# Kernel tuning notes

Hardware: AMD Instinct MI355X
Metric: run time of the kernel (lower is better)

Reference implementation:

```python
import jax, jax.numpy as jnp
import numpy as np

B, N, E, H, ET = 1, 50000, 600000, 128, 8
EPS = 1e-5


def setup_inputs() -> dict:
    key = jax.random.key(0)
    ks = jax.random.split(key, 20)
    s = 1.0 / np.sqrt(H)
    s2 = 1.0 / np.sqrt(2 * H)
    u = lambda k, shape, b: jax.random.uniform(k, shape, jnp.float32, -b, b)
    return {
        "hidden": jax.random.normal(ks[0], (B, N, H), jnp.float32),
        "edge_index": jax.random.randint(ks[1], (2, E), 0, N),
        "edge_type": jax.random.randint(ks[2], (E,), 0, ET),
        "edge_emb": jax.random.normal(ks[3], (ET, H), jnp.float32),
        "Wq": u(ks[4], (H, H), s), "bq": u(ks[5], (H,), s),
        "Wk": u(ks[6], (H, H), s), "bk": u(ks[7], (H,), s),
        "Wv": u(ks[8], (H, H), s), "bv": u(ks[9], (H,), s),
        "Web": u(ks[10], (H, 1), s), "beb": u(ks[11], (1,), s),
        "W1": u(ks[12], (2 * H, H), s2), "b1": u(ks[13], (H,), s2),
        "W2": u(ks[14], (H, H), s), "b2": u(ks[15], (H,), s),
        "gamma": jnp.ones((H,), jnp.float32),
        "beta": jnp.zeros((H,), jnp.float32),
    }


def reference(hidden, edge_index, edge_type, edge_emb, Wq, bq, Wk, bk, Wv, bv,
              Web, beb, W1, b1, W2, b2, gamma, beta):
    source, target = edge_index[0], edge_index[1]
    src_h = hidden[:, source]                      # [B,E,H] gather
    tgt_h = hidden[:, target]                      # [B,E,H] gather
    eh = edge_emb[edge_type]                       # [E,H]

    q = tgt_h @ Wq + bq                            # [B,E,H]
    sk = src_h + eh[None]                          # [B,E,H]
    k = sk @ Wk + bk
    v = sk @ Wv + bv

    logits = (q * k).sum(-1) / np.sqrt(H)          # [B,E]
    logits = logits + (eh @ Web + beb)[:, 0][None] # edge bias, same across batch

    # segment softmax over incoming edges per target node
    lt = logits.T                                  # [E,B]
    mx = jax.ops.segment_max(lt, target, num_segments=N)   # [N,B]
    ex = jnp.exp(lt - mx[target])
    sm = jax.ops.segment_sum(ex, target, num_segments=N)   # [N,B]
    w = (ex / sm[target]).T                        # [B,E]

    messages = v * w[..., None]                    # [B,E,H]
    agg = jax.ops.segment_sum(jnp.moveaxis(messages, 1, 0), target,
                              num_segments=N)      # [N,B,H]
    agg = jnp.moveaxis(agg, 0, 1)                  # [B,N,H]

    h = jnp.concatenate([hidden, agg], axis=-1)    # [B,N,2H]
    upd = jax.nn.silu(h @ W1 + b1) @ W2 + b2

    x = hidden + upd
    mu = x.mean(-1, keepdims=True)
    var = ((x - mu) ** 2).mean(-1, keepdims=True)
    return (x - mu) / jnp.sqrt(var + EPS) * gamma + beta
```

## Files before the change

kernel.cpp:

```cpp
#include <hip/hip_runtime.h>
#include <math.h>

#define NN 50000
#define NPAD 50048
#define NE 600000
#define H 128
#define ET 8
#define EPS 1e-5f
#define INVSQ 0.08838834764831845f

typedef __attribute__((ext_vector_type(8))) short bf16x8;
typedef __attribute__((ext_vector_type(8))) unsigned short u16x8;
typedef __attribute__((ext_vector_type(4))) float f32x4;

static __device__ inline float bf_lo(unsigned int w) { return __uint_as_float(w << 16); }
static __device__ inline float bf_hi(unsigned int w) { return __uint_as_float(w & 0xFFFF0000u); }
static __device__ inline float bfu(unsigned short v) {
  return __uint_as_float((unsigned int)v << 16);
}
static __device__ inline unsigned short f2bf(float f) {
  unsigned int u = __float_as_uint(f);
  return (unsigned short)((u + 0x7FFFu + ((u >> 16) & 1u)) >> 16);
}

#define PH_B 3125
#define PW_B 384
#define ET_B 8
#define HIST_B 2344

__global__ __launch_bounds__(256) void prep_all_kernel(
    const float* __restrict__ hidden, const float* __restrict__ edge_emb,
    const float* __restrict__ Wq, const float* __restrict__ Wk, const float* __restrict__ Wv,
    const float* __restrict__ W1, const float* __restrict__ W2,
    const float* __restrict__ Web, const float* __restrict__ beb,
    const int* __restrict__ tgt,
    unsigned short* __restrict__ hcat, unsigned short* __restrict__ WqkvT,
    unsigned short* __restrict__ W1T, unsigned short* __restrict__ W2T,
    float* __restrict__ Kef, float* __restrict__ Vef, float* __restrict__ ebuf,
    int* __restrict__ deg) {
  const int blk = blockIdx.x;
  const int t = threadIdx.x;
  if (blk < PH_B) {
    int g = blk * 256 + t;
    int row = g >> 4, seg = g & 15;
    const float4* src = (const float4*)(hidden + (size_t)row * 128 + seg * 8);
    float4 x0 = src[0], x1 = src[1];
    u16x8 o;
    o[0] = f2bf(x0.x); o[1] = f2bf(x0.y); o[2] = f2bf(x0.z); o[3] = f2bf(x0.w);
    o[4] = f2bf(x1.x); o[5] = f2bf(x1.y); o[6] = f2bf(x1.z); o[7] = f2bf(x1.w);
    *(u16x8*)(hcat + (size_t)row * 256 + seg * 8) = o;
  } else if (blk < PH_B + PW_B) {
    int idx = (blk - PH_B) * 256 + t;
    if (idx < 49152) {
      int r = idx >> 7, k = idx & 127;
      const float* W = (r < 128) ? Wq : (r < 256) ? Wk : Wv;
      WqkvT[idx] = f2bf(W[k * 128 + (r & 127)]);
    } else if (idx < 81920) {
      int j = idx - 49152;
      int r = j >> 8, k = j & 255;
      W1T[j] = f2bf(W1[k * 128 + r]);
    } else if (idx < 98304) {
      int j = idx - 81920;
      int r = j >> 7, k = j & 127;
      W2T[j] = f2bf(W2[k * 128 + r]);
    }
  } else if (blk < PH_B + PW_B + ET_B) {
    int e = blk - (PH_B + PW_B);
    if (t < 128) {
      float sk = 0.f, sv = 0.f;
      for (int i = 0; i < 128; ++i) {
        float ev = edge_emb[e * 128 + i];
        sk = fmaf(ev, Wk[i * 128 + t], sk);
        sv = fmaf(ev, Wv[i * 128 + t], sv);
      }
      Kef[e * 128 + t] = sk;
      Vef[e * 128 + t] = sv;
    } else if (t == 128) {
      float s2 = beb[0];
      for (int i = 0; i < 128; ++i) s2 = fmaf(edge_emb[e * 128 + i], Web[i], s2);
      ebuf[e] = s2;
    }
  } else {
    int e = (blk - (PH_B + PW_B + ET_B)) * 256 + t;
    if (e < NE) atomicAdd(&deg[tgt[e]], 1);
  }
}

__global__ __launch_bounds__(256) void qkv_mfma_kernel(
    const unsigned short* __restrict__ hcat, const unsigned short* __restrict__ WqkvT,
    const float* __restrict__ bq, const float* __restrict__ bk, const float* __restrict__ bv,
    unsigned short* __restrict__ Qb, unsigned short* __restrict__ KV_u16) {
  __shared__ unsigned short stage[64][392];
  const int tid = threadIdx.x;
  const int w = tid >> 6, l = tid & 63;
  const int lr = l & 15, lg = l >> 4;
  const int blk = blockIdx.x;

  f32x4 acc[4][6] = {};
  const unsigned short* Ab = hcat + (size_t)(blk * 64 + lr) * 256 + lg * 8;
  const unsigned short* Bb = WqkvT + (size_t)(w * 96 + lr) * 128 + lg * 8;
#pragma unroll
  for (int ks = 0; ks < 4; ++ks) {
    bf16x8 a[4];
#pragma unroll
    for (int mt = 0; mt < 4; ++mt) a[mt] = *(const bf16x8*)(Ab + mt * 16 * 256 + ks * 32);
#pragma unroll
    for (int ct = 0; ct < 6; ++ct) {
      bf16x8 b = *(const bf16x8*)(Bb + ct * 16 * 128 + ks * 32);
#pragma unroll
      for (int mt = 0; mt < 4; ++mt)
        acc[mt][ct] = __builtin_amdgcn_mfma_f32_16x16x32_bf16(a[mt], b, acc[mt][ct], 0, 0, 0);
    }
  }
#pragma unroll
  for (int ct = 0; ct < 6; ++ct) {
    int c = w * 96 + ct * 16 + lr;
    float bias = (c < 128) ? bq[c] : (c < 256) ? bk[c - 128] : bv[c - 256];
    float sc = (c < 128) ? INVSQ : 1.f;
    int off;
    if (c < 128) off = c;
    else if (c < 256) { int j = c - 128; off = 128 + ((j >> 1) << 2) + (j & 1); }
    else { int j = c - 256; off = 128 + ((j >> 1) << 2) + 2 + (j & 1); }
#pragma unroll
    for (int mt = 0; mt < 4; ++mt)
#pragma unroll
      for (int j = 0; j < 4; ++j)
        stage[mt * 16 + lg * 4 + j][off] = f2bf((acc[mt][ct][j] + bias) * sc);
  }
  __syncthreads();
  for (int idx = tid; idx < 64 * 48; idx += 256) {
    int r = idx / 48, g = idx % 48;
    int row = blk * 64 + r;
    if (row >= NN) continue;
    u16x8 v = *(const u16x8*)(&stage[r][g * 8]);
    if (g < 16) *(u16x8*)(Qb + (size_t)row * 128 + g * 8) = v;
    else *(u16x8*)(KV_u16 + (size_t)row * 256 + (g - 16) * 8) = v;
  }
}

__global__ __launch_bounds__(256) void qke_kernel(const unsigned short* __restrict__ Qb,
                                                  const float* __restrict__ Kef,
                                                  const float* __restrict__ ebuf,
                                                  float* __restrict__ qke) {
  const int wid = (blockIdx.x * 256 + threadIdx.x) >> 6;
  const int lane = threadIdx.x & 63;
  const int et = lane >> 3, part = lane & 7;
  const unsigned short* q = Qb + (size_t)wid * 128 + part * 16;
  u16x8 q0 = *(const u16x8*)q;
  u16x8 q1 = *(const u16x8*)(q + 8);
  const float4* kf = (const float4*)(Kef + et * 128 + part * 16);
  float4 k0 = kf[0], k1 = kf[1], k2 = kf[2], k3 = kf[3];
  float d = 0.f;
  d = fmaf(bfu(q0[0]), k0.x, d); d = fmaf(bfu(q0[1]), k0.y, d);
  d = fmaf(bfu(q0[2]), k0.z, d); d = fmaf(bfu(q0[3]), k0.w, d);
  d = fmaf(bfu(q0[4]), k1.x, d); d = fmaf(bfu(q0[5]), k1.y, d);
  d = fmaf(bfu(q0[6]), k1.z, d); d = fmaf(bfu(q0[7]), k1.w, d);
  d = fmaf(bfu(q1[0]), k2.x, d); d = fmaf(bfu(q1[1]), k2.y, d);
  d = fmaf(bfu(q1[2]), k2.z, d); d = fmaf(bfu(q1[3]), k2.w, d);
  d = fmaf(bfu(q1[4]), k3.x, d); d = fmaf(bfu(q1[5]), k3.y, d);
  d = fmaf(bfu(q1[6]), k3.z, d); d = fmaf(bfu(q1[7]), k3.w, d);
#pragma unroll
  for (int o = 4; o >= 1; o >>= 1) d += __shfl_xor(d, o);
  if (part == 0) qke[(size_t)wid * 8 + et] = d + ebuf[et];
}

__global__ __launch_bounds__(256) void scan1_kernel(const int* __restrict__ deg,
                                                    int* __restrict__ excl,
                                                    int* __restrict__ sums) {
  __shared__ int buf[256];
  int idx = blockIdx.x * 256 + threadIdx.x;
  int v = (idx < NN) ? deg[idx] : 0;
  buf[threadIdx.x] = v;
  __syncthreads();
  for (int o = 1; o < 256; o <<= 1) {
    int tv = (threadIdx.x >= o) ? buf[threadIdx.x - o] : 0;
    __syncthreads();
    buf[threadIdx.x] += tv;
    __syncthreads();
  }
  if (idx < NN) excl[idx] = buf[threadIdx.x] - v;
  if (threadIdx.x == 255) sums[blockIdx.x] = buf[255];
}

__global__ __launch_bounds__(256) void scan2_kernel(int* __restrict__ sums, int nb) {
  __shared__ int buf[256];
  int v = (threadIdx.x < nb) ? sums[threadIdx.x] : 0;
  buf[threadIdx.x] = v;
  __syncthreads();
  for (int o = 1; o < 256; o <<= 1) {
    int tv = (threadIdx.x >= o) ? buf[threadIdx.x - o] : 0;
    __syncthreads();
    buf[threadIdx.x] += tv;
    __syncthreads();
  }
  if (threadIdx.x < nb) sums[threadIdx.x] = buf[threadIdx.x] - v;
}

__global__ __launch_bounds__(256) void scan3_kernel(const int* __restrict__ excl,
                                                    const int* __restrict__ sums,
                                                    int* __restrict__ row_off,
                                                    int* __restrict__ cursor) {
  int idx = blockIdx.x * 256 + threadIdx.x;
  if (idx < NN) {
    int r = excl[idx] + sums[blockIdx.x];
    row_off[idx] = r;
    cursor[idx] = r;
  }
  if (idx == 0) row_off[NN] = NE;
}

__global__ void scatter_kernel(const int* __restrict__ src, const int* __restrict__ tgt,
                               const int* __restrict__ et, int* __restrict__ cursor,
                               int* __restrict__ packed) {
  int e = blockIdx.x * blockDim.x + threadIdx.x;
  if (e < NE) {
    int pos = atomicAdd(&cursor[tgt[e]], 1);
    packed[pos] = src[e] | (et[e] << 16);
  }
}

__global__ __launch_bounds__(256) void attn_kernel(
    const unsigned short* __restrict__ Qb, const uint4* __restrict__ KV4,
    const float* __restrict__ qke, const float* __restrict__ Vef,
    const int* __restrict__ row_off, const int* __restrict__ packed,
    unsigned short* __restrict__ hcat_u16) {
  const int wid = (blockIdx.x * blockDim.x + threadIdx.x) >> 6;
  const int lane = threadIdx.x & 63;
  const int g = lane >> 4, m = lane & 15;
  const int beg = row_off[wid], end = row_off[wid + 1];
  u16x8 qv = *(const u16x8*)(Qb + (size_t)wid * 128 + m * 8);
  float q[8];
#pragma unroll
  for (int j = 0; j < 8; ++j) q[j] = bfu(qv[j]);
  const float* qkb = qke + (size_t)wid * 8;
  float a[8] = {0.f, 0.f, 0.f, 0.f, 0.f, 0.f, 0.f, 0.f};
  float s = 0.f;
  for (int i = beg; i < end; i += 4) {
    int ii = i + g;
    bool valid = ii < end;
    int p = packed[valid ? ii : beg];
    int src = p & 0xFFFF, et = p >> 16;
    const uint4* row = KV4 + (size_t)src * 32 + m * 2;
    uint4 x0 = row[0], x1 = row[1];
    float d;
    d = bf_lo(x0.x) * q[0];
    d = fmaf(bf_hi(x0.x), q[1], d);
    d = fmaf(bf_lo(x0.z), q[2], d);
    d = fmaf(bf_hi(x0.z), q[3], d);
    d = fmaf(bf_lo(x1.x), q[4], d);
    d = fmaf(bf_hi(x1.x), q[5], d);
    d = fmaf(bf_lo(x1.z), q[6], d);
    d = fmaf(bf_hi(x1.z), q[7], d);
#pragma unroll
    for (int o = 8; o >= 1; o >>= 1) d += __shfl_xor(d, o);
    float pe = __expf(d + qkb[et]);
    pe = valid ? pe : 0.f;
    s += pe;
    const float4* vef = (const float4*)(Vef + et * 128 + m * 8);
    float4 v0 = vef[0], v1 = vef[1];
    a[0] = fmaf(pe, bf_lo(x0.y) + v0.x, a[0]);
    a[1] = fmaf(pe, bf_hi(x0.y) + v0.y, a[1]);
    a[2] = fmaf(pe, bf_lo(x0.w) + v0.z, a[2]);
    a[3] = fmaf(pe, bf_hi(x0.w) + v0.w, a[3]);
    a[4] = fmaf(pe, bf_lo(x1.y) + v1.x, a[4]);
    a[5] = fmaf(pe, bf_hi(x1.y) + v1.y, a[5]);
    a[6] = fmaf(pe, bf_lo(x1.w) + v1.z, a[6]);
    a[7] = fmaf(pe, bf_hi(x1.w) + v1.w, a[7]);
  }
#pragma unroll
  for (int o = 16; o <= 32; o <<= 1) {
    s += __shfl_xor(s, o);
#pragma unroll
    for (int j = 0; j < 8; ++j) a[j] += __shfl_xor(a[j], o);
  }
  if (g == 0) {
    float inv = (s > 0.f) ? 1.f / s : 0.f;
    u16x8 o;
#pragma unroll
    for (int j = 0; j < 8; ++j) o[j] = f2bf(a[j] * inv);
    *(u16x8*)(hcat_u16 + (size_t)wid * 256 + 128 + m * 8) = o;
  }
}

__global__ __launch_bounds__(256) void ffn_mfma_kernel(
    const unsigned short* __restrict__ hcat, const float* __restrict__ hidden,
    const unsigned short* __restrict__ W1T, const unsigned short* __restrict__ W2T,
    const float* __restrict__ b1, const float* __restrict__ b2,
    const float* __restrict__ gamma, const float* __restrict__ beta,
    float* __restrict__ out) {
  __shared__ unsigned short mid[64][136];
  const int tid = threadIdx.x;
  const int w = tid >> 6, l = tid & 63;
  const int lr = l & 15, lg = l >> 4;
  const int m0 = blockIdx.x * 64 + w * 16;

  f32x4 acc[8] = {};
  const unsigned short* Ab = hcat + (size_t)(m0 + lr) * 256 + lg * 8;
  const unsigned short* Bb = W1T + (size_t)lr * 256 + lg * 8;
#pragma unroll
  for (int ks = 0; ks < 8; ++ks) {
    bf16x8 a = *(const bf16x8*)(Ab + ks * 32);
#pragma unroll
    for (int ct = 0; ct < 8; ++ct) {
      bf16x8 b = *(const bf16x8*)(Bb + ct * 16 * 256 + ks * 32);
      acc[ct] = __builtin_amdgcn_mfma_f32_16x16x32_bf16(a, b, acc[ct], 0, 0, 0);
    }
  }
#pragma unroll
  for (int ct = 0; ct < 8; ++ct) {
    int c = ct * 16 + lr;
    float bb = b1[c];
#pragma unroll
    for (int j = 0; j < 4; ++j) {
      float x = acc[ct][j] + bb;
      float sl = x / (1.f + __expf(-x));
      mid[w * 16 + lg * 4 + j][c] = f2bf(sl);
    }
  }
  __syncthreads();

  f32x4 acc2[8] = {};
  const unsigned short* A2 = &mid[w * 16 + lr][0] + lg * 8;
  const unsigned short* B2 = W2T + (size_t)lr * 128 + lg * 8;
#pragma unroll
  for (int ks = 0; ks < 4; ++ks) {
    bf16x8 a = *(const bf16x8*)(A2 + ks * 32);
#pragma unroll
    for (int ct = 0; ct < 8; ++ct) {
      bf16x8 b = *(const bf16x8*)(B2 + ct * 16 * 128 + ks * 32);
      acc2[ct] = __builtin_amdgcn_mfma_f32_16x16x32_bf16(a, b, acc2[ct], 0, 0, 0);
    }
  }

  float ga[8], be[8], x[8][4];
#pragma unroll
  for (int ct = 0; ct < 8; ++ct) {
    int c = ct * 16 + lr;
    ga[ct] = gamma[c];
    be[ct] = beta[c];
    float bb = b2[c];
#pragma unroll
    for (int j = 0; j < 4; ++j) {
      int r = m0 + lg * 4 + j;
      float h = (r < NN) ? hidden[(size_t)r * 128 + c] : 0.f;
      x[ct][j] = acc2[ct][j] + bb + h;
    }
  }
#pragma unroll
  for (int j = 0; j < 4; ++j) {
    float s = 0.f, ss = 0.f;
#pragma unroll
    for (int ct = 0; ct < 8; ++ct) {
      s += x[ct][j];
      ss += x[ct][j] * x[ct][j];
    }
#pragma unroll
    for (int o = 8; o >= 1; o >>= 1) {
      s += __shfl_xor(s, o);
      ss += __shfl_xor(ss, o);
    }
    float mu = s * (1.f / 128.f);
    float inv = rsqrtf(ss * (1.f / 128.f) - mu * mu + EPS);
    int r = m0 + lg * 4 + j;
    if (r < NN) {
#pragma unroll
      for (int ct = 0; ct < 8; ++ct) {
        int c = ct * 16 + lr;
        out[(size_t)r * 128 + c] = (x[ct][j] - mu) * inv * ga[ct] + be[ct];
      }
    }
  }
}

extern "C" void kernel_launch(void* const* d_in, const int* in_sizes, int n_in,
                              void* d_out, int out_size, void* d_ws, size_t ws_size,
                              hipStream_t stream) {
  const float* hidden = (const float*)d_in[0];
  const int* edge_index = (const int*)d_in[1];
  const int* edge_type = (const int*)d_in[2];
  const float* edge_emb = (const float*)d_in[3];
  const float* Wq = (const float*)d_in[4];
  const float* bq = (const float*)d_in[5];
  const float* Wk = (const float*)d_in[6];
  const float* bk = (const float*)d_in[7];
  const float* Wv = (const float*)d_in[8];
  const float* bv = (const float*)d_in[9];
  const float* Web = (const float*)d_in[10];
  const float* beb = (const float*)d_in[11];
  const float* W1 = (const float*)d_in[12];
  const float* b1 = (const float*)d_in[13];
  const float* W2 = (const float*)d_in[14];
  const float* b2 = (const float*)d_in[15];
  const float* gamma = (const float*)d_in[16];
  const float* beta = (const float*)d_in[17];
  float* out = (float*)d_out;

  const int* srcp = edge_index;
  const int* tgtp = edge_index + NE;

  size_t off = 0;
  auto alloc = [&](size_t bytes) {
    void* p = (char*)d_ws + off;
    off += (bytes + 255) & ~(size_t)255;
    return p;
  };
  unsigned short* hcat = (unsigned short*)alloc((size_t)NPAD * 256 * 2);
  unsigned short* Qb = (unsigned short*)alloc((size_t)NPAD * 128 * 2);
  unsigned short* KV = (unsigned short*)alloc((size_t)NPAD * 256 * 2);
  unsigned short* WqkvT = (unsigned short*)alloc(384 * 128 * 2);
  unsigned short* W1T = (unsigned short*)alloc(128 * 256 * 2);
  unsigned short* W2T = (unsigned short*)alloc(128 * 128 * 2);
  float* Kef = (float*)alloc(ET * H * 4);
  float* Vef = (float*)alloc(ET * H * 4);
  float* ebuf = (float*)alloc(ET * 4);
  float* qke = (float*)alloc((size_t)NN * 8 * 4);
  int* deg = (int*)alloc((size_t)NN * 4);
  int* excl = (int*)alloc((size_t)NN * 4);
  int* sums = (int*)alloc(256 * 4);
  int* row_off = (int*)alloc((size_t)(NN + 1) * 4);
  int* cursor = (int*)alloc((size_t)NN * 4);
  int* packed = (int*)alloc((size_t)NE * 4);

  hipMemsetAsync(deg, 0, (size_t)NN * 4, stream);

  const int scan_blocks = (NN + 255) / 256;

  prep_all_kernel<<<PH_B + PW_B + ET_B + HIST_B, 256, 0, stream>>>(
      hidden, edge_emb, Wq, Wk, Wv, W1, W2, Web, beb, tgtp, hcat, WqkvT, W1T, W2T, Kef, Vef,
      ebuf, deg);
  scan1_kernel<<<scan_blocks, 256, 0, stream>>>(deg, excl, sums);
  scan2_kernel<<<1, 256, 0, stream>>>(sums, scan_blocks);
  scan3_kernel<<<scan_blocks, 256, 0, stream>>>(excl, sums, row_off, cursor);
  scatter_kernel<<<(NE + 255) / 256, 256, 0, stream>>>(srcp, tgtp, edge_type, cursor, packed);
  qkv_mfma_kernel<<<NPAD / 64, 256, 0, stream>>>(hcat, WqkvT, bq, bk, bv, Qb, KV);
  qke_kernel<<<NN / 4, 256, 0, stream>>>(Qb, Kef, ebuf, qke);
  attn_kernel<<<(NN * 64) / 256, 256, 0, stream>>>(Qb, (const uint4*)KV, qke, Vef, row_off,
                                                   packed, hcat);
  ffn_mfma_kernel<<<NPAD / 64, 256, 0, stream>>>(hcat, hidden, W1T, W2T, b1, b2, gamma, beta,
                                                 out);
}
```

Baseline: 333.3 us.

## Persistent FFN kernel with LDS-staged swizzled weights; split QKV tile across 8 waves

The FFN kernel becomes persistent with 256 blocks of 512 threads. Each block loads W1 and W2 once into swizzled LDS and its waves loop over 16-row tiles, each using a per-wave mid buffer. This removes the repeated global and L2 weight reads every block did before. The QKV kernel moves to 512 threads, with each wave computing a 32x96 tile instead of 64x96, which lowers register pressure and gives more waves per tile. The trade-off is about 100KB of LDS per FFN block, which limits occupancy, plus an explicit lgkmcnt wait in place of a block barrier.

```diff
diff --git a/kernel.cpp b/kernel.cpp
--- a/kernel.cpp
+++ b/kernel.cpp
@@ -3,6 +3,7 @@
 
 #define NN 50000
 #define NPAD 50048
+#define NTILES 3128
 #define NE 600000
 #define H 128
 #define ET 8
@@ -86,35 +87,34 @@
   }
 }
 
-__global__ __launch_bounds__(256) void qkv_mfma_kernel(
+__global__ __launch_bounds__(512) void qkv_mfma_kernel(
     const unsigned short* __restrict__ hcat, const unsigned short* __restrict__ WqkvT,
     const float* __restrict__ bq, const float* __restrict__ bk, const float* __restrict__ bv,
     unsigned short* __restrict__ Qb, unsigned short* __restrict__ KV_u16) {
   __shared__ unsigned short stage[64][392];
   const int tid = threadIdx.x;
   const int w = tid >> 6, l = tid & 63;
+  const int wr = w >> 2, wc = w & 3;
   const int lr = l & 15, lg = l >> 4;
   const int blk = blockIdx.x;
 
-  f32x4 acc[4][6] = {};
-  const unsigned short* Ab = hcat + (size_t)(blk * 64 + lr) * 256 + lg * 8;
-  const unsigned short* Bb = WqkvT + (size_t)(w * 96 + lr) * 128 + lg * 8;
+  f32x4 acc[2][6] = {};
+  const unsigned short* Ab = hcat + (size_t)(blk * 64 + wr * 32 + lr) * 256 + lg * 8;
+  const unsigned short* Bb = WqkvT + (size_t)(wc * 96 + lr) * 128 + lg * 8;
 #pragma unroll
   for (int ks = 0; ks < 4; ++ks) {
-    bf16x8 a[4];
-#pragma unroll
-    for (int mt = 0; mt < 4; ++mt) a[mt] = *(const bf16x8*)(Ab + mt * 16 * 256 + ks * 32);
+    bf16x8 a0 = *(const bf16x8*)(Ab + ks * 32);
+    bf16x8 a1 = *(const bf16x8*)(Ab + 16 * 256 + ks * 32);
 #pragma unroll
     for (int ct = 0; ct < 6; ++ct) {
       bf16x8 b = *(const bf16x8*)(Bb + ct * 16 * 128 + ks * 32);
-#pragma unroll
-      for (int mt = 0; mt < 4; ++mt)
-        acc[mt][ct] = __builtin_amdgcn_mfma_f32_16x16x32_bf16(a[mt], b, acc[mt][ct], 0, 0, 0);
+      acc[0][ct] = __builtin_amdgcn_mfma_f32_16x16x32_bf16(a0, b, acc[0][ct], 0, 0, 0);
+      acc[1][ct] = __builtin_amdgcn_mfma_f32_16x16x32_bf16(a1, b, acc[1][ct], 0, 0, 0);
     }
   }
 #pragma unroll
   for (int ct = 0; ct < 6; ++ct) {
-    int c = w * 96 + ct * 16 + lr;
+    int c = wc * 96 + ct * 16 + lr;
     float bias = (c < 128) ? bq[c] : (c < 256) ? bk[c - 128] : bv[c - 256];
     float sc = (c < 128) ? INVSQ : 1.f;
     int off;
@@ -122,13 +122,13 @@
     else if (c < 256) { int j = c - 128; off = 128 + ((j >> 1) << 2) + (j & 1); }
     else { int j = c - 256; off = 128 + ((j >> 1) << 2) + 2 + (j & 1); }
 #pragma unroll
-    for (int mt = 0; mt < 4; ++mt)
+    for (int mt = 0; mt < 2; ++mt)
 #pragma unroll
       for (int j = 0; j < 4; ++j)
-        stage[mt * 16 + lg * 4 + j][off] = f2bf((acc[mt][ct][j] + bias) * sc);
+        stage[wr * 32 + mt * 16 + lg * 4 + j][off] = f2bf((acc[mt][ct][j] + bias) * sc);
   }
   __syncthreads();
-  for (int idx = tid; idx < 64 * 48; idx += 256) {
+  for (int idx = tid; idx < 64 * 48; idx += 512) {
     int r = idx / 48, g = idx % 48;
     int row = blk * 64 + r;
     if (row >= NN) continue;
@@ -282,91 +282,128 @@
   }
 }
 
-__global__ __launch_bounds__(256) void ffn_mfma_kernel(
+__global__ __launch_bounds__(512) void ffn_mfma_kernel(
     const unsigned short* __restrict__ hcat, const float* __restrict__ hidden,
     const unsigned short* __restrict__ W1T, const unsigned short* __restrict__ W2T,
     const float* __restrict__ b1, const float* __restrict__ b2,
     const float* __restrict__ gamma, const float* __restrict__ beta,
     float* __restrict__ out) {
-  __shared__ unsigned short mid[64][136];
+  __shared__ unsigned short w1s[32768];
+  __shared__ unsigned short w2s[16384];
+  __shared__ unsigned short mids[8][2176];
   const int tid = threadIdx.x;
   const int w = tid >> 6, l = tid & 63;
   const int lr = l & 15, lg = l >> 4;
-  const int m0 = blockIdx.x * 64 + w * 16;
-
-  f32x4 acc[8] = {};
-  const unsigned short* Ab = hcat + (size_t)(m0 + lr) * 256 + lg * 8;
-  const unsigned short* Bb = W1T + (size_t)lr * 256 + lg * 8;
-#pragma unroll
-  for (int ks = 0; ks < 8; ++ks) {
-    bf16x8 a = *(const bf16x8*)(Ab + ks * 32);
-#pragma unroll
-    for (int ct = 0; ct < 8; ++ct) {
-      bf16x8 b = *(const bf16x8*)(Bb + ct * 16 * 256 + ks * 32);
-      acc[ct] = __builtin_amdgcn_mfma_f32_16x16x32_bf16(a, b, acc[ct], 0, 0, 0);
-    }
-  }
+
+#pragma unroll
+  for (int it = 0; it < 8; ++it) {
+    int idx = it * 512 + tid;
+    int c = idx >> 5, ks8 = idx & 31;
+    u16x8 v = *(const u16x8*)(W1T + c * 256 + ks8 * 8);
+    int byte = (c * 512 + ks8 * 16) ^ ((c & 7) << 4);
+    *(u16x8*)((char*)w1s + byte) = v;
+  }
+#pragma unroll
+  for (int it = 0; it < 4; ++it) {
+    int idx = it * 512 + tid;
+    int c = idx >> 4, ks8 = idx & 15;
+    u16x8 v = *(const u16x8*)(W2T + c * 128 + ks8 * 8);
+    int byte = (c * 256 + ks8 * 16) ^ ((c & 7) << 4);
+    *(u16x8*)((char*)w2s + byte) = v;
+  }
+  __syncthreads();
+
+  float bias1[8], bias2[8], ga[8], be[8];
 #pragma unroll
   for (int ct = 0; ct < 8; ++ct) {
     int c = ct * 16 + lr;
-    float bb = b1[c];
-#pragma unroll
-    for (int j = 0; j < 4; ++j) {
-      float x = acc[ct][j] + bb;
-      float sl = x / (1.f + __expf(-x));
-      mid[w * 16 + lg * 4 + j][c] = f2bf(sl);
-    }
-  }
-  __syncthreads();
-
-  f32x4 acc2[8] = {};
-  const unsigned short* A2 = &mid[w * 16 + lr][0] + lg * 8;
-  const unsigned short* B2 = W2T + (size_t)lr * 128 + lg * 8;
-#pragma unroll
-  for (int ks = 0; ks < 4; ++ks) {
-    bf16x8 a = *(const bf16x8*)(A2 + ks * 32);
-#pragma unroll
-    for (int ct = 0; ct < 8; ++ct) {
-      bf16x8 b = *(const bf16x8*)(B2 + ct * 16 * 128 + ks * 32);
-      acc2[ct] = __builtin_amdgcn_mfma_f32_16x16x32_bf16(a, b, acc2[ct], 0, 0, 0);
-    }
-  }
-
-  float ga[8], be[8], x[8][4];
-#pragma unroll
-  for (int ct = 0; ct < 8; ++ct) {
-    int c = ct * 16 + lr;
+    bias1[ct] = b1[c];
+    bias2[ct] = b2[c];
     ga[ct] = gamma[c];
     be[ct] = beta[c];
-    float bb = b2[c];
+  }
+  unsigned short* midw = mids[w];
+  const char* w1b = (const char*)w1s;
+  const char* w2b = (const char*)w2s;
+
+  for (int t = blockIdx.x * 8 + w; t < NTILES; t += 2048) {
+    const unsigned short* Ab = hcat + (size_t)(t * 16 + lr) * 256 + lg * 8;
+    bf16x8 a[8];
+#pragma unroll
+    for (int ks = 0; ks < 8; ++ks) a[ks] = *(const bf16x8*)(Ab + ks * 32);
+
+    f32x4 acc[8] = {};
+#pragma unroll
+    for (int ks = 0; ks < 8; ++ks) {
+#pragma unroll
+      for (int ct = 0; ct < 8; ++ct) {
+        int byte = ((ct * 16 + lr) * 512 + (lg * 8 + ks * 32) * 2) ^ ((lr & 7) << 4);
+        bf16x8 b = *(const bf16x8*)(w1b + byte);
+        acc[ct] = __builtin_amdgcn_mfma_f32_16x16x32_bf16(a[ks], b, acc[ct], 0, 0, 0);
+      }
+    }
+
+    float res[8][4];
+#pragma unroll
+    for (int ct = 0; ct < 8; ++ct)
+#pragma unroll
+      for (int j = 0; j < 4; ++j) {
+        int r = t * 16 + lg * 4 + j;
+        res[ct][j] = (r < NN) ? hidden[(size_t)r * 128 + ct * 16 + lr] : 0.f;
+      }
+
+#pragma unroll
+    for (int ct = 0; ct < 8; ++ct) {
+      float bb = bias1[ct];
+#pragma unroll
+      for (int j = 0; j < 4; ++j) {
+        float x = acc[ct][j] + bb;
+        float sl = x / (1.f + __expf(-x));
+        midw[(lg * 4 + j) * 136 + ct * 16 + lr] = f2bf(sl);
+      }
+    }
+    asm volatile("s_waitcnt lgkmcnt(0)" ::: "memory");
+    __builtin_amdgcn_sched_barrier(0);
+
+    f32x4 acc2[8] = {};
+#pragma unroll
+    for (int ks = 0; ks < 4; ++ks) {
+      bf16x8 a2 = *(const bf16x8*)(midw + lr * 136 + lg * 8 + ks * 32);
+#pragma unroll
+      for (int ct = 0; ct < 8; ++ct) {
+        int byte = ((ct * 16 + lr) * 256 + (lg * 8 + ks * 32) * 2) ^ ((lr & 7) << 4);
+        bf16x8 b = *(const bf16x8*)(w2b + byte);
+        acc2[ct] = __builtin_amdgcn_mfma_f32_16x16x32_bf16(a2, b, acc2[ct], 0, 0, 0);
+      }
+    }
+
+    float x[8][4];
+#pragma unroll
+    for (int ct = 0; ct < 8; ++ct)
+#pragma unroll
+      for (int j = 0; j < 4; ++j) x[ct][j] = acc2[ct][j] + bias2[ct] + res[ct][j];
 #pragma unroll
     for (int j = 0; j < 4; ++j) {
-      int r = m0 + lg * 4 + j;
-      float h = (r < NN) ? hidden[(size_t)r * 128 + c] : 0.f;
-      x[ct][j] = acc2[ct][j] + bb + h;
-    }
-  }
-#pragma unroll
-  for (int j = 0; j < 4; ++j) {
-    float s = 0.f, ss = 0.f;
-#pragma unroll
-    for (int ct = 0; ct < 8; ++ct) {
-      s += x[ct][j];
-      ss += x[ct][j] * x[ct][j];
-    }
-#pragma unroll
-    for (int o = 8; o >= 1; o >>= 1) {
-      s += __shfl_xor(s, o);
-      ss += __shfl_xor(ss, o);
-    }
-    float mu = s * (1.f / 128.f);
-    float inv = rsqrtf(ss * (1.f / 128.f) - mu * mu + EPS);
-    int r = m0 + lg * 4 + j;
-    if (r < NN) {
+      float s = 0.f, ss = 0.f;
 #pragma unroll
       for (int ct = 0; ct < 8; ++ct) {
-        int c = ct * 16 + lr;
-        out[(size_t)r * 128 + c] = (x[ct][j] - mu) * inv * ga[ct] + be[ct];
+        s += x[ct][j];
+        ss += x[ct][j] * x[ct][j];
+      }
+#pragma unroll
+      for (int o = 8; o >= 1; o >>= 1) {
+        s += __shfl_xor(s, o);
+        ss += __shfl_xor(ss, o);
+      }
+      float mu = s * (1.f / 128.f);
+      float inv = rsqrtf(ss * (1.f / 128.f) - mu * mu + EPS);
+      int r = t * 16 + lg * 4 + j;
+      if (r < NN) {
+#pragma unroll
+        for (int ct = 0; ct < 8; ++ct) {
+          int c = ct * 16 + lr;
+          out[(size_t)r * 128 + c] = (x[ct][j] - mu) * inv * ga[ct] + be[ct];
+        }
       }
     }
   }
@@ -432,10 +469,9 @@
   scan2_kernel<<<1, 256, 0, stream>>>(sums, scan_blocks);
   scan3_kernel<<<scan_blocks, 256, 0, stream>>>(excl, sums, row_off, cursor);
   scatter_kernel<<<(NE + 255) / 256, 256, 0, stream>>>(srcp, tgtp, edge_type, cursor, packed);
-  qkv_mfma_kernel<<<NPAD / 64, 256, 0, stream>>>(hcat, WqkvT, bq, bk, bv, Qb, KV);
+  qkv_mfma_kernel<<<NPAD / 64, 512, 0, stream>>>(hcat, WqkvT, bq, bk, bv, Qb, KV);
   qke_kernel<<<NN / 4, 256, 0, stream>>>(Qb, Kef, ebuf, qke);
   attn_kernel<<<(NN * 64) / 256, 256, 0, stream>>>(Qb, (const uint4*)KV, qke, Vef, row_off,
                                                    packed, hcat);
-  ffn_mfma_kernel<<<NPAD / 64, 256, 0, stream>>>(hcat, hidden, W1T, W2T, b1, b2, gamma, beta,
-                                                 out);
-}
+  ffn_mfma_kernel<<<256, 512, 0, stream>>>(hcat, hidden, W1T, W2T, b1, b2, gamma, beta, out);
+}
```

Result: faster. 296.7 us (-11.0%).
